# Kernel optimization log

Hardware: AMD Instinct MI355X
Metric: run time of the kernel (lower is better)

The kernel has to match this reference:

```python
import jax, jax.numpy as jnp
import numpy as np

N_NODES = 100000
N_EDGES = 1000000
D = 64
LN_EPS = 1e-5
DIV_EPS = 1e-6


def _layernorm(x, g, b):
    mu = x.mean(-1, keepdims=True)
    var = ((x - mu) ** 2).mean(-1, keepdims=True)
    return (x - mu) * jax.lax.rsqrt(var + LN_EPS) * g + b


def _linear_params(key, d_in, d_out):
    kw, kb = jax.random.split(key)
    s = 1.0 / np.sqrt(d_in)
    w = jax.random.uniform(kw, (d_in, d_out), jnp.float32, -s, s)
    b = jax.random.uniform(kb, (d_out,), jnp.float32, -s, s)
    return w, b


def setup_inputs() -> dict:
    key = jax.random.key(0)
    ks = jax.random.split(key, 10)
    h = jax.random.normal(ks[0], (N_NODES, D), jnp.float32)
    e = jax.random.normal(ks[1], (N_EDGES, D), jnp.float32)
    src = jax.random.randint(ks[2], (N_EDGES,), 0, N_NODES)
    dst = jax.random.randint(ks[3], (N_EDGES,), 0, N_NODES)
    A1w, A1b = _linear_params(ks[4], D, D)
    A2w, A2b = _linear_params(ks[5], D, D)
    B1w, B1b = _linear_params(ks[6], D, D)
    B2w, B2b = _linear_params(ks[7], D, D)
    B3w, B3b = _linear_params(ks[8], D, D)
    return {
        "h": h, "e": e, "src": src, "dst": dst,
        "A1w": A1w, "A1b": A1b, "A2w": A2w, "A2b": A2b,
        "B1w": B1w, "B1b": B1b, "B2w": B2w, "B2b": B2b,
        "B3w": B3w, "B3b": B3b,
        "ln_e_g": jnp.ones((D,), jnp.float32), "ln_e_b": jnp.zeros((D,), jnp.float32),
        "ln_h_g": jnp.ones((D,), jnp.float32), "ln_h_b": jnp.zeros((D,), jnp.float32),
    }


def reference(h, e, src, dst, A1w, A1b, A2w, A2b, B1w, B1b, B2w, B2b, B3w, B3b,
              ln_e_g, ln_e_b, ln_h_g, ln_h_b):
    # dense projections (small GEMMs, d=64)
    A1h = h @ A1w + A1b          # [N, D]
    A2h = h @ A2w + A2b          # [N, D]
    B1h = h @ B1w + B1b          # [N, D]
    B2h = h @ B2w + B2b          # [N, D]
    B3e = e @ B3w + B3b          # [E, D]

    # apply_edges u_add_v: B1h[src] + B2h[dst], plus B3e
    e_ji = B1h[src] + B2h[dst] + B3e            # [E, D]
    e_ji = jax.nn.relu(_layernorm(e_ji, ln_e_g, ln_e_b))
    e_ji = e_ji + e                              # residual (in==out)

    sigma = jax.nn.sigmoid(e_ji)                 # [E, D]

    # update_all u_mul_e sum: sum over incoming edges at dst of A2h[src]*sigma
    sum_sigma_h = jax.ops.segment_sum(A2h[src] * sigma, dst, num_segments=N_NODES)
    sum_sigma = jax.ops.segment_sum(sigma, dst, num_segments=N_NODES)

    h_forward = sum_sigma_h / (sum_sigma + DIV_EPS)
    h_out = jax.nn.relu(_layernorm(A1h + h_forward, ln_h_g, ln_h_b))
    h_out = h_out + h                            # residual
    return (h_out, e_ji)
```

## Files before the change

kernel.cpp:

```cpp
#include <hip/hip_runtime.h>

#define D 64
#define LN_EPS 1e-5f
#define DIV_EPS 1e-6f

typedef __attribute__((ext_vector_type(8))) short bf16x8;
typedef __attribute__((ext_vector_type(4))) float f32x4;

__device__ __forceinline__ short f2bf(float f) {
  unsigned u = __float_as_uint(f);
  unsigned r = (u + 0x7fffu + ((u >> 16) & 1u)) >> 16;
  return (short)r;
}

__device__ __forceinline__ f32x4 ntld4(const float* p) {
  return __builtin_nontemporal_load((const f32x4*)p);
}

__device__ __forceinline__ float gsum16(float v) {
#pragma unroll
  for (int m = 1; m < 16; m <<= 1) v += __shfl_xor(v, m, 64);
  return v;
}

__device__ __forceinline__ bf16x8 load_bfrag(const float* __restrict__ W,
                                             int s, int n0, int lane) {
  const int c = n0 * 16 + (lane & 15);
  const int k0 = s * 32 + ((lane >> 4) << 3);
  bf16x8 b;
#pragma unroll
  for (int j = 0; j < 8; ++j) b[j] = f2bf(W[(k0 + j) * D + c]);
  return b;
}

__device__ __forceinline__ void load_afrags(const float* __restrict__ X,
                                            size_t r0, int lane, bf16x8& a0,
                                            bf16x8& a1) {
  const int q = lane >> 4, m = lane & 15;
  const float* rb = X + (r0 + m) * D;
  const float4* p0 = (const float4*)(rb + q * 8);
  const float4* p1 = (const float4*)(rb + 32 + q * 8);
  float4 v0 = p0[0], v1 = p0[1], v2 = p1[0], v3 = p1[1];
  a0 = (bf16x8){f2bf(v0.x), f2bf(v0.y), f2bf(v0.z), f2bf(v0.w),
                f2bf(v1.x), f2bf(v1.y), f2bf(v1.z), f2bf(v1.w)};
  a1 = (bf16x8){f2bf(v2.x), f2bf(v2.y), f2bf(v2.z), f2bf(v2.w),
                f2bf(v3.x), f2bf(v3.y), f2bf(v3.z), f2bf(v3.w)};
}

__global__ __launch_bounds__(256, 1) void node_proj_mfma(
    const float* __restrict__ h, const float* __restrict__ W0,
    const float* __restrict__ Bb0, const float* __restrict__ W1,
    const float* __restrict__ Bb1, const float* __restrict__ W2,
    const float* __restrict__ Bb2, const float* __restrict__ W3,
    const float* __restrict__ Bb3, float* __restrict__ o0,
    float* __restrict__ o1, float* __restrict__ o2, float* __restrict__ o3,
    int N) {
  const int lane = threadIdx.x & 63;
  const int q = lane >> 4, m = lane & 15;
  const int wave = blockIdx.x * 4 + (threadIdx.x >> 6);
  const int nw = gridDim.x * 4;
  const float* Ws[4] = {W0, W1, W2, W3};
  const float* Bs[4] = {Bb0, Bb1, Bb2, Bb3};
  float* Os[4] = {o0, o1, o2, o3};
  bf16x8 bf[4][2][4];
  float bias[4][4];
#pragma unroll
  for (int mat = 0; mat < 4; ++mat) {
#pragma unroll
    for (int s = 0; s < 2; ++s)
#pragma unroll
      for (int n0 = 0; n0 < 4; ++n0)
        bf[mat][s][n0] = load_bfrag(Ws[mat], s, n0, lane);
#pragma unroll
    for (int n0 = 0; n0 < 4; ++n0) bias[mat][n0] = Bs[mat][n0 * 16 + m];
  }
  for (int r0 = wave * 16; r0 < N; r0 += nw * 16) {
    bf16x8 a0, a1;
    load_afrags(h, (size_t)r0, lane, a0, a1);
#pragma unroll
    for (int mat = 0; mat < 4; ++mat) {
      f32x4 acc[4];
#pragma unroll
      for (int n0 = 0; n0 < 4; ++n0) {
        acc[n0] = (f32x4){0.f, 0.f, 0.f, 0.f};
        acc[n0] = __builtin_amdgcn_mfma_f32_16x16x32_bf16(a0, bf[mat][0][n0],
                                                          acc[n0], 0, 0, 0);
        acc[n0] = __builtin_amdgcn_mfma_f32_16x16x32_bf16(a1, bf[mat][1][n0],
                                                          acc[n0], 0, 0, 0);
      }
      float* Om = Os[mat];
#pragma unroll
      for (int n0 = 0; n0 < 4; ++n0)
#pragma unroll
        for (int r = 0; r < 4; ++r)
          Om[(size_t)(r0 + q * 4 + r) * D + n0 * 16 + m] =
              acc[n0][r] + bias[mat][n0];
    }
  }
}

__global__ __launch_bounds__(256, 3) void edge_mfma3(
    const float* __restrict__ e, const int* __restrict__ src,
    const int* __restrict__ dst, const float* __restrict__ B1h,
    const float* __restrict__ B2h, const float* __restrict__ A2h,
    const float* __restrict__ W3, const float* __restrict__ B3b,
    const float* __restrict__ g, const float* __restrict__ bta,
    float* __restrict__ eout, float* __restrict__ ssh, float* __restrict__ ss,
    int E) {
  __shared__ float es[4][16][68];
  const int lane = threadIdx.x & 63;
  const int q = lane >> 4, m = lane & 15;
  const int wid = threadIdx.x >> 6;
  const int gw = blockIdx.x * 4 + wid;
  const int nw = gridDim.x * 4;
  bf16x8 bf[2][4];
#pragma unroll
  for (int s = 0; s < 2; ++s)
#pragma unroll
    for (int n0 = 0; n0 < 4; ++n0) bf[s][n0] = load_bfrag(W3, s, n0, lane);
  float bb[4], gl[4], bl[4];
#pragma unroll
  for (int k = 0; k < 4; ++k) {
    const int c = m + 16 * k;
    bb[k] = B3b[c];
    gl[k] = g[c];
    bl[k] = bta[c];
  }
  for (int e0 = gw * 16; e0 < E; e0 += nw * 16) {
    const float* rb = e + (size_t)(e0 + m) * D;
    f32x4 v0 = ntld4(rb + q * 8);
    f32x4 v1 = ntld4(rb + q * 8 + 4);
    f32x4 v2 = ntld4(rb + 32 + q * 8);
    f32x4 v3 = ntld4(rb + 32 + q * 8 + 4);
    f32x4* erow = (f32x4*)&es[wid][m][0];
    erow[q * 2] = v0;
    erow[q * 2 + 1] = v1;
    erow[8 + q * 2] = v2;
    erow[8 + q * 2 + 1] = v3;
    bf16x8 a0 = (bf16x8){f2bf(v0[0]), f2bf(v0[1]), f2bf(v0[2]), f2bf(v0[3]),
                         f2bf(v1[0]), f2bf(v1[1]), f2bf(v1[2]), f2bf(v1[3])};
    bf16x8 a1 = (bf16x8){f2bf(v2[0]), f2bf(v2[1]), f2bf(v2[2]), f2bf(v2[3]),
                         f2bf(v3[0]), f2bf(v3[1]), f2bf(v3[2]), f2bf(v3[3])};
    f32x4 acc[4];
#pragma unroll
    for (int n0 = 0; n0 < 4; ++n0) {
      acc[n0] = (f32x4){0.f, 0.f, 0.f, 0.f};
      acc[n0] =
          __builtin_amdgcn_mfma_f32_16x16x32_bf16(a0, bf[0][n0], acc[n0], 0, 0, 0);
      acc[n0] =
          __builtin_amdgcn_mfma_f32_16x16x32_bf16(a1, bf[1][n0], acc[n0], 0, 0, 0);
    }
    const int sv = src[e0 + m];
    const int dv = dst[e0 + m];
#pragma unroll
    for (int r = 0; r < 4; ++r) {
      const int tr = q * 4 + r;
      const int sN = __shfl(sv, tr, 64);
      const int dN = __shfl(dv, tr, 64);
      const size_t sb = (size_t)sN * D, db = (size_t)dN * D;
      float x[4], a2[4], part = 0.f;
#pragma unroll
      for (int k = 0; k < 4; ++k) {
        const int c = m + 16 * k;
        x[k] = acc[k][r] + bb[k] + B1h[sb + c] + B2h[db + c];
        a2[k] = A2h[sb + c];
        part += x[k];
      }
      const float mu = gsum16(part) * (1.f / 64.f);
      float dx[4], vp = 0.f;
#pragma unroll
      for (int k = 0; k < 4; ++k) {
        dx[k] = x[k] - mu;
        vp += dx[k] * dx[k];
      }
      const float rs = rsqrtf(gsum16(vp) * (1.f / 64.f) + LN_EPS);
      const size_t eb = (size_t)(e0 + tr) * D;
#pragma unroll
      for (int k = 0; k < 4; ++k) {
        const int c = m + 16 * k;
        float y = fmaxf(dx[k] * rs * gl[k] + bl[k], 0.f) + es[wid][tr][c];
        __builtin_nontemporal_store(y, eout + eb + c);
        const float sg = 1.f / (1.f + __expf(-y));
        atomicAdd(&ssh[db + c], a2[k] * sg);
        atomicAdd(&ss[db + c], sg);
      }
    }
  }
}

__global__ __launch_bounds__(256) void node_out2(
    const float* __restrict__ h, const float* __restrict__ A1h,
    const float* __restrict__ ssh, const float* __restrict__ ss,
    const float* __restrict__ g, const float* __restrict__ bta,
    float* __restrict__ hout, int n) {
  const int lane = threadIdx.x & 63;
  const int q = lane >> 4, m = lane & 15;
  const int wave = blockIdx.x * 4 + (threadIdx.x >> 6);
  const int nw = gridDim.x * 4;
  const f32x4 gl = ((const f32x4*)g)[m];
  const f32x4 bl = ((const f32x4*)bta)[m];
  for (int n0 = wave * 4; n0 < n; n0 += nw * 4) {
    const int row = n0 + q;
    if (row >= n) continue;
    const size_t base = (size_t)row * D + m * 4;
    f32x4 a1 = ntld4(A1h + base);
    f32x4 s1 = ntld4(ssh + base);
    f32x4 s2 = ntld4(ss + base);
    f32x4 hv = ntld4(h + base);
    float x[4], part = 0.f;
#pragma unroll
    for (int k = 0; k < 4; ++k) {
      x[k] = a1[k] + s1[k] / (s2[k] + DIV_EPS);
      part += x[k];
    }
    const float mu = gsum16(part) * (1.f / 64.f);
    float dx[4], vp = 0.f;
#pragma unroll
    for (int k = 0; k < 4; ++k) {
      dx[k] = x[k] - mu;
      vp += dx[k] * dx[k];
    }
    const float rs = rsqrtf(gsum16(vp) * (1.f / 64.f) + LN_EPS);
    f32x4 y;
#pragma unroll
    for (int k = 0; k < 4; ++k)
      y[k] = fmaxf(dx[k] * rs * gl[k] + bl[k], 0.f) + hv[k];
    __builtin_nontemporal_store(y, (f32x4*)(hout + base));
  }
}

extern "C" void kernel_launch(void* const* d_in, const int* in_sizes, int n_in,
                              void* d_out, int out_size, void* d_ws,
                              size_t ws_size, hipStream_t stream) {
  const float* h = (const float*)d_in[0];
  const float* e = (const float*)d_in[1];
  const int* src = (const int*)d_in[2];
  const int* dst = (const int*)d_in[3];
  const float* A1w = (const float*)d_in[4];
  const float* A1b = (const float*)d_in[5];
  const float* A2w = (const float*)d_in[6];
  const float* A2b = (const float*)d_in[7];
  const float* B1w = (const float*)d_in[8];
  const float* B1b = (const float*)d_in[9];
  const float* B2w = (const float*)d_in[10];
  const float* B2b = (const float*)d_in[11];
  const float* B3w = (const float*)d_in[12];
  const float* B3b = (const float*)d_in[13];
  const float* ln_e_g = (const float*)d_in[14];
  const float* ln_e_b = (const float*)d_in[15];
  const float* ln_h_g = (const float*)d_in[16];
  const float* ln_h_b = (const float*)d_in[17];

  const int N = in_sizes[0] / D;
  const int E = in_sizes[1] / D;

  float* ws = (float*)d_ws;
  float* A1h = ws;
  float* A2h = ws + (size_t)N * D;
  float* B1h = ws + 2 * (size_t)N * D;
  float* B2h = ws + 3 * (size_t)N * D;
  float* ssh = ws + 4 * (size_t)N * D;
  float* ss = ws + 5 * (size_t)N * D;

  float* hout = (float*)d_out;
  float* eout = (float*)d_out + (size_t)N * D;

  hipMemsetAsync(ssh, 0, 2 * (size_t)N * D * sizeof(float), stream);

  node_proj_mfma<<<1563, 256, 0, stream>>>(h, B1w, B1b, B2w, B2b, A1w, A1b,
                                           A2w, A2b, B1h, B2h, A1h, A2h, N);
  edge_mfma3<<<3907, 256, 0, stream>>>(e, src, dst, B1h, B2h, A2h, B3w, B3b,
                                       ln_e_g, ln_e_b, eout, ssh, ss, E);
  node_out2<<<2048, 256, 0, stream>>>(h, A1h, ssh, ss, ln_h_g, ln_h_b, hout, N);
}
```

Baseline: 865.4 us.

## Replace atomic scatter aggregation with CSR-by-destination gather in fused output kernel

Builds a destination-sorted edge list each call (histogram, three-pass scan, atomic placement) and moves the sigmoid-weighted aggregation into the node output kernel, which gathers each node's incoming edges from the written edge output and A2h. This drops the 128M float atomics and the big zero memset of the two accumulator buffers. The cost is extra gather reads of edge outputs and A2h, plus five small launches. The node projection is also split so each wave handles one weight matrix, trading more blocks for fewer registers.

```diff
diff --git a/kernel.cpp b/kernel.cpp
--- a/kernel.cpp
+++ b/kernel.cpp
@@ -47,7 +47,7 @@
                 f2bf(v3.x), f2bf(v3.y), f2bf(v3.z), f2bf(v3.w)};
 }
 
-__global__ __launch_bounds__(256, 1) void node_proj_mfma(
+__global__ __launch_bounds__(256) void node_proj2(
     const float* __restrict__ h, const float* __restrict__ W0,
     const float* __restrict__ Bb0, const float* __restrict__ W1,
     const float* __restrict__ Bb1, const float* __restrict__ W2,
@@ -57,56 +57,114 @@
     int N) {
   const int lane = threadIdx.x & 63;
   const int q = lane >> 4, m = lane & 15;
-  const int wave = blockIdx.x * 4 + (threadIdx.x >> 6);
-  const int nw = gridDim.x * 4;
+  const int wid = threadIdx.x >> 6;
   const float* Ws[4] = {W0, W1, W2, W3};
   const float* Bs[4] = {Bb0, Bb1, Bb2, Bb3};
   float* Os[4] = {o0, o1, o2, o3};
-  bf16x8 bf[4][2][4];
-  float bias[4][4];
-#pragma unroll
-  for (int mat = 0; mat < 4; ++mat) {
-#pragma unroll
-    for (int s = 0; s < 2; ++s)
-#pragma unroll
-      for (int n0 = 0; n0 < 4; ++n0)
-        bf[mat][s][n0] = load_bfrag(Ws[mat], s, n0, lane);
-#pragma unroll
-    for (int n0 = 0; n0 < 4; ++n0) bias[mat][n0] = Bs[mat][n0 * 16 + m];
-  }
-  for (int r0 = wave * 16; r0 < N; r0 += nw * 16) {
+  const float* W = Ws[wid];
+  float* Om = Os[wid];
+  bf16x8 bf[2][4];
+#pragma unroll
+  for (int s = 0; s < 2; ++s)
+#pragma unroll
+    for (int n0 = 0; n0 < 4; ++n0) bf[s][n0] = load_bfrag(W, s, n0, lane);
+  float bias[4];
+#pragma unroll
+  for (int n0 = 0; n0 < 4; ++n0) bias[n0] = Bs[wid][n0 * 16 + m];
+  for (int r0 = blockIdx.x * 16; r0 < N; r0 += gridDim.x * 16) {
     bf16x8 a0, a1;
     load_afrags(h, (size_t)r0, lane, a0, a1);
-#pragma unroll
-    for (int mat = 0; mat < 4; ++mat) {
-      f32x4 acc[4];
-#pragma unroll
-      for (int n0 = 0; n0 < 4; ++n0) {
-        acc[n0] = (f32x4){0.f, 0.f, 0.f, 0.f};
-        acc[n0] = __builtin_amdgcn_mfma_f32_16x16x32_bf16(a0, bf[mat][0][n0],
-                                                          acc[n0], 0, 0, 0);
-        acc[n0] = __builtin_amdgcn_mfma_f32_16x16x32_bf16(a1, bf[mat][1][n0],
-                                                          acc[n0], 0, 0, 0);
-      }
-      float* Om = Os[mat];
-#pragma unroll
-      for (int n0 = 0; n0 < 4; ++n0)
-#pragma unroll
-        for (int r = 0; r < 4; ++r)
-          Om[(size_t)(r0 + q * 4 + r) * D + n0 * 16 + m] =
-              acc[n0][r] + bias[mat][n0];
-    }
-  }
-}
-
-__global__ __launch_bounds__(256, 3) void edge_mfma3(
+    f32x4 acc[4];
+#pragma unroll
+    for (int n0 = 0; n0 < 4; ++n0) {
+      acc[n0] = (f32x4){0.f, 0.f, 0.f, 0.f};
+      acc[n0] =
+          __builtin_amdgcn_mfma_f32_16x16x32_bf16(a0, bf[0][n0], acc[n0], 0, 0, 0);
+      acc[n0] =
+          __builtin_amdgcn_mfma_f32_16x16x32_bf16(a1, bf[1][n0], acc[n0], 0, 0, 0);
+    }
+#pragma unroll
+    for (int n0 = 0; n0 < 4; ++n0)
+#pragma unroll
+      for (int r = 0; r < 4; ++r)
+        Om[(size_t)(r0 + q * 4 + r) * D + n0 * 16 + m] = acc[n0][r] + bias[n0];
+  }
+}
+
+
+__global__ __launch_bounds__(256) void hist_kernel(const int* __restrict__ dst,
+                                                   int* __restrict__ cnt,
+                                                   int E) {
+  for (int i = blockIdx.x * blockDim.x + threadIdx.x; i < E;
+       i += gridDim.x * blockDim.x)
+    atomicAdd(&cnt[dst[i]], 1);
+}
+
+#define SCAN_B 256
+__global__ __launch_bounds__(SCAN_B) void scan1(const int* __restrict__ cnt,
+                                                int* __restrict__ rs,
+                                                int* __restrict__ bsum, int n) {
+  __shared__ int s[SCAN_B];
+  const int i = blockIdx.x * SCAN_B + threadIdx.x;
+  const int v = (i < n) ? cnt[i] : 0;
+  s[threadIdx.x] = v;
+  __syncthreads();
+#pragma unroll
+  for (int off = 1; off < SCAN_B; off <<= 1) {
+    int t = (threadIdx.x >= off) ? s[threadIdx.x - off] : 0;
+    __syncthreads();
+    s[threadIdx.x] += t;
+    __syncthreads();
+  }
+  if (i < n) rs[i] = s[threadIdx.x] - v;
+  if (threadIdx.x == SCAN_B - 1) bsum[blockIdx.x] = s[SCAN_B - 1];
+}
+
+__global__ __launch_bounds__(512) void scan2(int* __restrict__ bsum, int nb) {
+  __shared__ int s[512];
+  const int v = (threadIdx.x < nb) ? bsum[threadIdx.x] : 0;
+  s[threadIdx.x] = v;
+  __syncthreads();
+#pragma unroll
+  for (int off = 1; off < 512; off <<= 1) {
+    int t = (threadIdx.x >= off) ? s[threadIdx.x - off] : 0;
+    __syncthreads();
+    s[threadIdx.x] += t;
+    __syncthreads();
+  }
+  if (threadIdx.x < nb) bsum[threadIdx.x] = s[threadIdx.x] - v;
+}
+
+__global__ __launch_bounds__(SCAN_B) void scan3(int* __restrict__ rs,
+                                                int* __restrict__ cur,
+                                                const int* __restrict__ bsum,
+                                                int n, int E) {
+  const int i = blockIdx.x * SCAN_B + threadIdx.x;
+  if (i < n) {
+    const int v = rs[i] + bsum[blockIdx.x];
+    rs[i] = v;
+    cur[i] = v;
+  }
+  if (blockIdx.x == 0 && threadIdx.x == 0) rs[n] = E;
+}
+
+__global__ __launch_bounds__(256) void place_kernel(const int* __restrict__ dst,
+                                                    int* __restrict__ cur,
+                                                    int* __restrict__ list,
+                                                    int E) {
+  for (int i = blockIdx.x * blockDim.x + threadIdx.x; i < E;
+       i += gridDim.x * blockDim.x) {
+    const int p = atomicAdd(&cur[dst[i]], 1);
+    list[p] = i;
+  }
+}
+
+__global__ __launch_bounds__(256, 4) void edge_mfma4(
     const float* __restrict__ e, const int* __restrict__ src,
     const int* __restrict__ dst, const float* __restrict__ B1h,
-    const float* __restrict__ B2h, const float* __restrict__ A2h,
-    const float* __restrict__ W3, const float* __restrict__ B3b,
-    const float* __restrict__ g, const float* __restrict__ bta,
-    float* __restrict__ eout, float* __restrict__ ssh, float* __restrict__ ss,
-    int E) {
+    const float* __restrict__ B2h, const float* __restrict__ W3,
+    const float* __restrict__ B3b, const float* __restrict__ g,
+    const float* __restrict__ bta, float* __restrict__ eout, int E) {
   __shared__ float es[4][16][68];
   const int lane = threadIdx.x & 63;
   const int q = lane >> 4, m = lane & 15;
@@ -158,12 +216,11 @@
       const int sN = __shfl(sv, tr, 64);
       const int dN = __shfl(dv, tr, 64);
       const size_t sb = (size_t)sN * D, db = (size_t)dN * D;
-      float x[4], a2[4], part = 0.f;
+      float x[4], part = 0.f;
 #pragma unroll
       for (int k = 0; k < 4; ++k) {
         const int c = m + 16 * k;
         x[k] = acc[k][r] + bb[k] + B1h[sb + c] + B2h[db + c];
-        a2[k] = A2h[sb + c];
         part += x[k];
       }
       const float mu = gsum16(part) * (1.f / 64.f);
@@ -178,39 +235,52 @@
 #pragma unroll
       for (int k = 0; k < 4; ++k) {
         const int c = m + 16 * k;
-        float y = fmaxf(dx[k] * rs * gl[k] + bl[k], 0.f) + es[wid][tr][c];
-        __builtin_nontemporal_store(y, eout + eb + c);
-        const float sg = 1.f / (1.f + __expf(-y));
-        atomicAdd(&ssh[db + c], a2[k] * sg);
-        atomicAdd(&ss[db + c], sg);
+        eout[eb + c] = fmaxf(dx[k] * rs * gl[k] + bl[k], 0.f) + es[wid][tr][c];
       }
     }
   }
 }
 
-__global__ __launch_bounds__(256) void node_out2(
+__global__ __launch_bounds__(256) void aggregate_out(
     const float* __restrict__ h, const float* __restrict__ A1h,
-    const float* __restrict__ ssh, const float* __restrict__ ss,
-    const float* __restrict__ g, const float* __restrict__ bta,
-    float* __restrict__ hout, int n) {
+    const float* __restrict__ A2h, const float* __restrict__ eout,
+    const int* __restrict__ rs, const int* __restrict__ list,
+    const int* __restrict__ src, const float* __restrict__ g,
+    const float* __restrict__ bta, float* __restrict__ hout, int N) {
   const int lane = threadIdx.x & 63;
   const int q = lane >> 4, m = lane & 15;
   const int wave = blockIdx.x * 4 + (threadIdx.x >> 6);
   const int nw = gridDim.x * 4;
   const f32x4 gl = ((const f32x4*)g)[m];
   const f32x4 bl = ((const f32x4*)bta)[m];
-  for (int n0 = wave * 4; n0 < n; n0 += nw * 4) {
-    const int row = n0 + q;
-    if (row >= n) continue;
-    const size_t base = (size_t)row * D + m * 4;
-    f32x4 a1 = ntld4(A1h + base);
-    f32x4 s1 = ntld4(ssh + base);
-    f32x4 s2 = ntld4(ss + base);
-    f32x4 hv = ntld4(h + base);
+  for (int n = wave * 4 + q; n < N; n += nw * 4) {
+    const int s = rs[n], t = rs[n + 1];
+    f32x4 acc0 = (f32x4){0.f, 0.f, 0.f, 0.f};
+    f32x4 acc1 = (f32x4){0.f, 0.f, 0.f, 0.f};
+    for (int b = s; b < t; b += 16) {
+      const int nn = min(16, t - b);
+      const int jm = (m < nn) ? list[b + m] : 0;
+      const int sm = (m < nn) ? src[jm] : 0;
+      for (int u = 0; u < nn; ++u) {
+        const int jj = __shfl(jm, q * 16 + u, 64);
+        const int sj = __shfl(sm, q * 16 + u, 64);
+        const f32x4 y = *(const f32x4*)(eout + (size_t)jj * D + m * 4);
+        const f32x4 a2 = *(const f32x4*)(A2h + (size_t)sj * D + m * 4);
+#pragma unroll
+        for (int k = 0; k < 4; ++k) {
+          const float sg = 1.f / (1.f + __expf(-y[k]));
+          acc0[k] += sg;
+          acc1[k] += a2[k] * sg;
+        }
+      }
+    }
+    const size_t base = (size_t)n * D + m * 4;
+    const f32x4 a1 = ntld4(A1h + base);
+    const f32x4 hv = ntld4(h + base);
     float x[4], part = 0.f;
 #pragma unroll
     for (int k = 0; k < 4; ++k) {
-      x[k] = a1[k] + s1[k] / (s2[k] + DIV_EPS);
+      x[k] = a1[k] + acc1[k] / (acc0[k] + DIV_EPS);
       part += x[k];
     }
     const float mu = gsum16(part) * (1.f / 64.f);
@@ -220,11 +290,11 @@
       dx[k] = x[k] - mu;
       vp += dx[k] * dx[k];
     }
-    const float rs = rsqrtf(gsum16(vp) * (1.f / 64.f) + LN_EPS);
+    const float rsv = rsqrtf(gsum16(vp) * (1.f / 64.f) + LN_EPS);
     f32x4 y;
 #pragma unroll
     for (int k = 0; k < 4; ++k)
-      y[k] = fmaxf(dx[k] * rs * gl[k] + bl[k], 0.f) + hv[k];
+      y[k] = fmaxf(dx[k] * rsv * gl[k] + bl[k], 0.f) + hv[k];
     __builtin_nontemporal_store(y, (f32x4*)(hout + base));
   }
 }
@@ -259,17 +329,28 @@
   float* A2h = ws + (size_t)N * D;
   float* B1h = ws + 2 * (size_t)N * D;
   float* B2h = ws + 3 * (size_t)N * D;
-  float* ssh = ws + 4 * (size_t)N * D;
-  float* ss = ws + 5 * (size_t)N * D;
+  int* ip = (int*)(ws + 4 * (size_t)N * D);
+  int* rs = ip;
+  int* cur = ip + (N + 1);
+  int* list = cur + N;
+  int* bsum = list + E;
 
   float* hout = (float*)d_out;
   float* eout = (float*)d_out + (size_t)N * D;
 
-  hipMemsetAsync(ssh, 0, 2 * (size_t)N * D * sizeof(float), stream);
-
-  node_proj_mfma<<<1563, 256, 0, stream>>>(h, B1w, B1b, B2w, B2b, A1w, A1b,
-                                           A2w, A2b, B1h, B2h, A1h, A2h, N);
-  edge_mfma3<<<3907, 256, 0, stream>>>(e, src, dst, B1h, B2h, A2h, B3w, B3b,
-                                       ln_e_g, ln_e_b, eout, ssh, ss, E);
-  node_out2<<<2048, 256, 0, stream>>>(h, A1h, ssh, ss, ln_h_g, ln_h_b, hout, N);
-}
+  const int nb = (N + SCAN_B - 1) / SCAN_B;
+
+  hipMemsetAsync(cur, 0, (size_t)N * sizeof(int), stream);
+
+  node_proj2<<<3125, 256, 0, stream>>>(h, B1w, B1b, B2w, B2b, A1w, A1b, A2w,
+                                       A2b, B1h, B2h, A1h, A2h, N);
+  hist_kernel<<<512, 256, 0, stream>>>(dst, cur, E);
+  scan1<<<nb, SCAN_B, 0, stream>>>(cur, rs, bsum, N);
+  scan2<<<1, 512, 0, stream>>>(bsum, nb);
+  scan3<<<nb, SCAN_B, 0, stream>>>(rs, cur, bsum, N, E);
+  place_kernel<<<512, 256, 0, stream>>>(dst, cur, list, E);
+  edge_mfma4<<<3907, 256, 0, stream>>>(e, src, dst, B1h, B2h, B3w, B3b, ln_e_g,
+                                       ln_e_b, eout, E);
+  aggregate_out<<<4096, 256, 0, stream>>>(h, A1h, A2h, eout, rs, list, src,
+                                          ln_h_g, ln_h_b, hout, N);
+}
```

Result: faster. 793.5 us (-8.3%).
